# Kernel tuning notes

Hardware: AMD Instinct MI355X
Metric: run time of the kernel (lower is better)

Reference implementation:

```python
import jax, jax.numpy as jnp
import numpy as np
import math

B_, V_, D_, N_, H_, W_ = 4, 8, 64, 16, 32, 32
V_LIST = [0.0, 45.0, 90.0, 135.0, 180.0, 225.0, 270.0, 315.0]
GROUPS = 4
EPS = 1e-5


def _make_sample_coords():
    # Replicates F.affine_grid(align_corners=False) for fixed rotation matrices,
    # then maps normalized grid coords to input pixel coords as grid_sample does.
    xs = (np.arange(W_) + 0.5) * 2.0 / W_ - 1.0
    ys = (np.arange(H_) + 0.5) * 2.0 / H_ - 1.0
    X, Y = np.meshgrid(xs, ys)  # (H, W)
    ix_list, iy_list = [], []
    for w in V_LIST:
        a = math.radians(-w)
        c, s = math.cos(a), math.sin(a)
        gx = c * X - s * Y  # theta = [[c,-s,0],[s,c,0]]
        gy = s * X + c * Y
        ix_list.append((gx + 1.0) * W_ / 2.0 - 0.5)
        iy_list.append((gy + 1.0) * H_ / 2.0 - 0.5)
    return (jnp.asarray(np.stack(ix_list), jnp.float32),
            jnp.asarray(np.stack(iy_list), jnp.float32))

IX, IY = _make_sample_coords()  # each (V, H, W)


def _bilinear(sv, iy, ix):
    # sv: (B, D, N, H, W); iy, ix: (H, W) float sampling coords (pixel space)
    x0 = jnp.floor(ix)
    y0 = jnp.floor(iy)
    wx1 = ix - x0
    wy1 = iy - y0

    def corner(yc, xc, wgt):
        m = (yc >= 0) & (yc < H_) & (xc >= 0) & (xc < W_)  # zeros padding
        yi = jnp.clip(yc, 0, H_ - 1).astype(jnp.int32)
        xi = jnp.clip(xc, 0, W_ - 1).astype(jnp.int32)
        return sv[..., yi, xi] * jnp.where(m, wgt, 0.0)

    return (corner(y0, x0, (1.0 - wy1) * (1.0 - wx1))
            + corner(y0, x0 + 1.0, (1.0 - wy1) * wx1)
            + corner(y0 + 1.0, x0, wy1 * (1.0 - wx1))
            + corner(y0 + 1.0, x0 + 1.0, wy1 * wx1))

# vmap over the velocity axis V of s_prev and the per-velocity grids
_transport = jax.vmap(_bilinear, in_axes=(1, 0, 0), out_axes=1)


def _conv(x, w, b=None):
    y = jax.lax.conv_general_dilated(x, w, (1, 1), 'SAME',
                                     dimension_numbers=('NCHW', 'OIHW', 'NCHW'))
    if b is not None:
        y = y + b[None, :, None, None]
    return y


def _group_norm(x, w, b):
    Bn, D, H, W = x.shape
    xg = x.reshape(Bn, GROUPS, D // GROUPS, H, W)
    mu = xg.mean(axis=(2, 3, 4), keepdims=True)
    var = xg.var(axis=(2, 3, 4), keepdims=True)
    xn = ((xg - mu) * jax.lax.rsqrt(var + EPS)).reshape(Bn, D, H, W)
    return xn * w[None, :, None, None] + b[None, :, None, None]


def setup_inputs() -> dict:
    key = jax.random.key(0)
    ks = jax.random.split(key, 5)
    return {
        "u_t": jax.random.normal(ks[0], (B_, D_, H_, W_), jnp.float32),
        "s_prev": jax.random.normal(ks[1], (B_, V_, D_, N_, H_, W_), jnp.float32) * 0.1,
        "gn_w": jnp.ones((D_,), jnp.float32),
        "gn_b": jnp.zeros((D_,), jnp.float32),
        "conv_delta_w": jax.random.normal(ks[2], (D_, D_, 3, 3), jnp.float32) * 0.02,
        "conv_delta_b": jnp.zeros((D_,), jnp.float32),
        "conv_B_w": jax.random.normal(ks[3], (N_, D_, 3, 3), jnp.float32) * 0.02,
        "conv_C_w": jax.random.normal(ks[4], (N_, D_, 3, 3), jnp.float32) * 0.02,
        "log_A_real": jnp.full((D_, N_), math.log(0.5), jnp.float32),
        "D_param": jnp.ones((D_,), jnp.float32),
        "dt_bias": jnp.float32(math.log(math.e - 1.0)),
    }


def reference(u_t, s_prev, gn_w, gn_b, conv_delta_w, conv_delta_b,
              conv_B_w, conv_C_w, log_A_real, D_param, dt_bias):
    u_norm = _group_norm(u_t, gn_w, gn_b)
    delta = jax.nn.softplus(_conv(u_norm, conv_delta_w, conv_delta_b) + dt_bias)
    delta = jnp.clip(delta, 1e-4, 5.0)                               # (B,D,H,W)
    B_val = _conv(u_norm, conv_B_w)                                  # (B,N,H,W)
    C_val = _conv(u_norm, conv_C_w)                                  # (B,N,H,W)
    A = -jnp.exp(log_A_real)                                         # (D,N)
    A_bar = jnp.exp(delta[:, :, None] * A[None, :, :, None, None])   # (B,D,N,H,W)
    B_bar = delta[:, :, None] * B_val[:, None]                       # (B,D,N,H,W)
    s_trans = _transport(s_prev, IY, IX)                             # (B,V,D,N,H,W)
    s_new = A_bar[:, None] * s_trans + B_bar[:, None] * u_t[:, None, :, None]
    y_state = jnp.einsum('bvdnhw,bnhw->bvdhw', s_new, C_val)
    y_new = y_state + u_t[:, None] * D_param[None, None, :, None, None]
    return (y_new, s_new)
```

## Files before the change

kernel.cpp:

```cpp
#include <hip/hip_runtime.h>
#include <cmath>

#define FSQ 0.70710678118654752440f
__constant__ float CTAB[8] = {1.f,  FSQ, 0.f, -FSQ, -1.f, -FSQ, 0.f, FSQ};
__constant__ float STAB[8] = {0.f, -FSQ, -1.f, -FSQ,  0.f,  FSQ, 1.f, FSQ};

__global__ __launch_bounds__(256) void gn_kernel(const float* __restrict__ u,
                                                 const float* __restrict__ gw,
                                                 const float* __restrict__ gb,
                                                 float* __restrict__ up)
{
    int blk = blockIdx.x;
    int b = blk >> 2, g = blk & 3;
    int t = threadIdx.x;
    const float* src = u + ((size_t)(b * 64 + g * 16) << 10);
    float sum = 0.f, sq = 0.f;
    #pragma unroll
    for (int r = 0; r < 64; ++r) {
        float v = src[t + (r << 8)];
        sum += v; sq += v * v;
    }
    __shared__ float red[256], red2[256];
    red[t] = sum; red2[t] = sq;
    __syncthreads();
    for (int ofs = 128; ofs > 0; ofs >>= 1) {
        if (t < ofs) { red[t] += red[t + ofs]; red2[t] += red2[t + ofs]; }
        __syncthreads();
    }
    float mu  = red[0] * (1.f / 16384.f);
    float var = red2[0] * (1.f / 16384.f) - mu * mu;
    float rs  = rsqrtf(var + 1e-5f);

    float* pb = up + (size_t)(b * 64 + g * 16) * 1156;
    for (int k = t; k < 16 * 132; k += 256) {
        int pl = k / 132, c = k % 132;
        int idx;
        if (c < 34)       idx = c;
        else if (c < 68)  idx = 33 * 34 + (c - 34);
        else if (c < 100) idx = (c - 68 + 1) * 34;
        else              idx = (c - 100 + 1) * 34 + 33;
        pb[pl * 1156 + idx] = 0.f;
    }
    for (int r = 0; r < 64; ++r) {
        int idx = t + (r << 8);
        int ch = idx >> 10, rem = idx & 1023;
        int y = rem >> 5, x = rem & 31;
        float val = (src[idx] - mu) * rs * gw[g * 16 + ch] + gb[g * 16 + ch];
        pb[ch * 1156 + (y + 1) * 34 + (x + 1)] = val;
    }
}

__global__ __launch_bounds__(256) void conv_kernel(const float* __restrict__ up,
                                                   const float* __restrict__ wd,
                                                   const float* __restrict__ bd,
                                                   const float* __restrict__ wB,
                                                   const float* __restrict__ wC,
                                                   const float* __restrict__ dtb,
                                                   float* __restrict__ delta,
                                                   float* __restrict__ Bv,
                                                   float* __restrict__ Cv)
{
    int blk = blockIdx.x;
    int o = blk % 96, b = blk / 96;
    int t = threadIdx.x;
    int w = t & 31, h0 = (t >> 5) << 2;
    const float* wsel;
    if (o < 64)      wsel = wd + (size_t)o * 576;
    else if (o < 80) wsel = wB + (size_t)(o - 64) * 576;
    else             wsel = wC + (size_t)(o - 80) * 576;
    const float* plane = up + (size_t)b * 64 * 1156;

    float acc[4] = {0.f, 0.f, 0.f, 0.f};
    for (int ci = 0; ci < 64; ++ci) {
        const float* pl = plane + ci * 1156 + h0 * 34 + w;
        const float* wp = wsel + ci * 9;
        float v[6][3];
        #pragma unroll
        for (int ry = 0; ry < 6; ++ry)
            #pragma unroll
            for (int dx = 0; dx < 3; ++dx)
                v[ry][dx] = pl[ry * 34 + dx];
        float w9[9];
        #pragma unroll
        for (int k = 0; k < 9; ++k) w9[k] = wp[k];
        #pragma unroll
        for (int r = 0; r < 4; ++r)
            #pragma unroll
            for (int dy = 0; dy < 3; ++dy)
                #pragma unroll
                for (int dx = 0; dx < 3; ++dx)
                    acc[r] += v[r + dy][dx] * w9[dy * 3 + dx];
    }

    int pbase = (h0 << 5) + w;
    if (o < 64) {
        float bias = bd[o] + dtb[0];
        float* dst = delta + ((size_t)(b * 64 + o) << 10) + pbase;
        #pragma unroll
        for (int r = 0; r < 4; ++r) {
            float x = acc[r] + bias;
            float sp = (x > 20.f) ? x : log1pf(expf(x));
            sp = fminf(fmaxf(sp, 1e-4f), 5.f);
            dst[r << 5] = sp;
        }
    } else {
        float* dst = (o < 80) ? (Bv + ((size_t)(b * 16 + o - 64) << 10) + pbase)
                              : (Cv + ((size_t)(b * 16 + o - 80) << 10) + pbase);
        #pragma unroll
        for (int r = 0; r < 4; ++r) dst[r << 5] = acc[r];
    }
}

__global__ __launch_bounds__(256) void fused_state_kernel(
    const float* __restrict__ s_prev, const float* __restrict__ u_t,
    const float* __restrict__ delta, const float* __restrict__ Bv,
    const float* __restrict__ Cv, const float* __restrict__ logA,
    const float* __restrict__ Dp, float* __restrict__ y_out,
    float* __restrict__ s_out)
{
    __shared__ float lds[8516];
    __shared__ float Ash[16];
    int blk = blockIdx.x;
    int d = blk & 63, v = (blk >> 6) & 7, b = blk >> 9;
    int t = threadIdx.x;

    if (t < 16) Ash[t] = -expf(logA[d * 16 + t]);
    for (int k = t; k < 324; k += 256) {
        int idx;
        if (k < 34)       idx = k;
        else if (k < 290) { int q = k - 34; idx = 34 + (q >> 5) * 1056 + (q & 31) * 33 + 32; }
        else              idx = 8482 + (k - 290);
        lds[idx] = 0.f;
    }

    const float cc = CTAB[v], ss = STAB[v];
    const float* dpl = delta + ((size_t)(b * 64 + d) << 10);
    const float* upl = u_t   + ((size_t)(b * 64 + d) << 10);

    float w00[4], w01[4], w10[4], w11[4], du[4], dl[4], uu[4], yacc[4];
    int base[4];
    #pragma unroll
    for (int i = 0; i < 4; ++i) {
        int p = t + (i << 8);
        int h = p >> 5, wpx = p & 31;
        float X = (wpx + 0.5f) * 0.0625f - 1.f;
        float Y = (h + 0.5f) * 0.0625f - 1.f;
        float gx = cc * X - ss * Y;
        float gy = ss * X + cc * Y;
        float ix = (gx + 1.f) * 16.f - 0.5f;
        float iy = (gy + 1.f) * 16.f - 0.5f;
        float fx0 = floorf(ix), fy0 = floorf(iy);
        float wx = ix - fx0, wy = iy - fy0;
        int x0 = (int)fx0, y0 = (int)fy0;
        bool vx0 = (x0 >= 0) && (x0 < 32);
        bool vx1 = (x0 >= -1) && (x0 < 31);
        bool vy0 = (y0 >= 0) && (y0 < 32);
        bool vy1 = (y0 >= -1) && (y0 < 31);
        float mx0 = vx0 ? (1.f - wx) : 0.f;
        float mx1 = vx1 ? wx : 0.f;
        float my0 = vy0 ? (1.f - wy) : 0.f;
        float my1 = vy1 ? wy : 0.f;
        w00[i] = my0 * mx0; w01[i] = my0 * mx1;
        w10[i] = my1 * mx0; w11[i] = my1 * mx1;
        int bx = min(max(x0, -1), 31), by = min(max(y0, -1), 31);
        base[i] = 34 + by * 33 + bx;
        float dd = dpl[p], uv = upl[p];
        dl[i] = dd; uu[i] = uv; du[i] = dd * uv; yacc[i] = 0.f;
    }

    size_t so = ((size_t)((b * 8 + v) * 64 + d)) << 14;
    const float* sb  = s_prev + so;
    float* sob = s_out + so;
    const float* BvB = Bv + ((size_t)b << 14);
    const float* CvB = Cv + ((size_t)b << 14);

    for (int ch = 0; ch < 2; ++ch) {
        const float4* src = (const float4*)(sb + (ch << 13));
        #pragma unroll
        for (int q0 = 0; q0 < 8; ++q0) {
            int q = t + (q0 << 8);
            float4 val = src[q];
            int lin = q << 2;
            int n = lin >> 10, rem = lin & 1023;
            int di = 34 + n * 1056 + (rem >> 5) * 33 + (rem & 31);
            lds[di] = val.x; lds[di + 1] = val.y; lds[di + 2] = val.z; lds[di + 3] = val.w;
        }
        __syncthreads();

        const float* bvc = BvB + (ch << 13);
        const float* cvc = CvB + (ch << 13);
        float* soc = sob + (ch << 13);
        #pragma unroll
        for (int i = 0; i < 4; ++i) {
            int p = t + (i << 8);
            #pragma unroll
            for (int n = 0; n < 8; ++n) {
                int si = base[i] + n * 1056;
                float s00 = lds[si], s01 = lds[si + 1];
                float s10 = lds[si + 33], s11 = lds[si + 34];
                float bil = s00 * w00[i] + s01 * w01[i] + s10 * w10[i] + s11 * w11[i];
                float abar = __expf(dl[i] * Ash[(ch << 3) + n]);
                float sn = abar * bil + du[i] * bvc[(n << 10) + p];
                soc[(n << 10) + p] = sn;
                yacc[i] += sn * cvc[(n << 10) + p];
            }
        }
        __syncthreads();
    }

    float Dd = Dp[d];
    float* yo = y_out + (((size_t)((b * 8 + v) * 64 + d)) << 10);
    #pragma unroll
    for (int i = 0; i < 4; ++i) {
        int p = t + (i << 8);
        yo[p] = yacc[i] + uu[i] * Dd;
    }
}

extern "C" void kernel_launch(void* const* d_in, const int* in_sizes, int n_in,
                              void* d_out, int out_size, void* d_ws, size_t ws_size,
                              hipStream_t stream)
{
    const float* u_t    = (const float*)d_in[0];
    const float* s_prev = (const float*)d_in[1];
    const float* gn_w   = (const float*)d_in[2];
    const float* gn_b   = (const float*)d_in[3];
    const float* wd     = (const float*)d_in[4];
    const float* bd     = (const float*)d_in[5];
    const float* wB     = (const float*)d_in[6];
    const float* wC     = (const float*)d_in[7];
    const float* logA   = (const float*)d_in[8];
    const float* Dp     = (const float*)d_in[9];
    const float* dtb    = (const float*)d_in[10];

    float* y_out = (float*)d_out;
    float* s_out = y_out + 2097152;

    float* up    = (float*)d_ws;
    float* delta = up + 295936;
    float* Bv    = delta + 262144;
    float* Cv    = Bv + 65536;

    hipLaunchKernelGGL(gn_kernel, dim3(16), dim3(256), 0, stream, u_t, gn_w, gn_b, up);
    hipLaunchKernelGGL(conv_kernel, dim3(384), dim3(256), 0, stream,
                       up, wd, bd, wB, wC, dtb, delta, Bv, Cv);
    hipLaunchKernelGGL(fused_state_kernel, dim3(2048), dim3(256), 0, stream,
                       s_prev, u_t, delta, Bv, Cv, logA, Dp, y_out, s_out);
}
```

Measured before the change: 346.5 us.

## Split conv into row strips with LDS staging and split state kernel over N

The conv kernel now launches one block per (batch, output channel, 4-row strip), stages the 6-row halo of all 64 input channels in shared memory, and splits the input-channel sum across two thread halves that are reduced through LDS. The fused state kernel is split into two blocks per (b,v,d), each handling 8 of the 16 state channels with a 34-wide padded LDS tile. The partial y sums are combined with atomicAdd into an output that is first zeroed by a memset. The aim is more parallelism and occupancy in both kernels, at the cost of an extra memset pass, atomic traffic on y, and repeated loading of the conv input per output channel.

```diff
diff --git a/kernel.cpp b/kernel.cpp
--- a/kernel.cpp
+++ b/kernel.cpp
@@ -60,54 +60,60 @@
                                                    float* __restrict__ Bv,
                                                    float* __restrict__ Cv)
 {
+    __shared__ float sin_[64 * 204];
+    __shared__ float red[256];
     int blk = blockIdx.x;
-    int o = blk % 96, b = blk / 96;
+    int strip = blk & 7;
+    int o = (blk >> 3) & 127; o = o % 96;
+    o = ((blk >> 3) - (blk / 768) * 96);
+    int b = blk / 768;
+    int h0 = strip * 4;
     int t = threadIdx.x;
-    int w = t & 31, h0 = (t >> 5) << 2;
+
+    const float* plane = up + (size_t)b * 73984;
+    for (int idx = t; idx < 13056; idx += 256) {
+        int ci = idx / 204;
+        int rem = idx - ci * 204;
+        sin_[idx] = plane[ci * 1156 + h0 * 34 + rem];
+    }
+    __syncthreads();
+
     const float* wsel;
     if (o < 64)      wsel = wd + (size_t)o * 576;
     else if (o < 80) wsel = wB + (size_t)(o - 64) * 576;
     else             wsel = wC + (size_t)(o - 80) * 576;
-    const float* plane = up + (size_t)b * 64 * 1156;
-
-    float acc[4] = {0.f, 0.f, 0.f, 0.f};
-    for (int ci = 0; ci < 64; ++ci) {
-        const float* pl = plane + ci * 1156 + h0 * 34 + w;
+
+    int half = t >> 7;
+    int px = t & 127;
+    int r = px >> 5, c = px & 31;
+    const float* base = sin_ + r * 34 + c;
+
+    float acc = 0.f;
+    int ci0 = half * 32;
+    for (int ci = ci0; ci < ci0 + 32; ++ci) {
+        const float* pp = base + ci * 204;
         const float* wp = wsel + ci * 9;
-        float v[6][3];
         #pragma unroll
-        for (int ry = 0; ry < 6; ++ry)
+        for (int dy = 0; dy < 3; ++dy)
             #pragma unroll
             for (int dx = 0; dx < 3; ++dx)
-                v[ry][dx] = pl[ry * 34 + dx];
-        float w9[9];
-        #pragma unroll
-        for (int k = 0; k < 9; ++k) w9[k] = wp[k];
-        #pragma unroll
-        for (int r = 0; r < 4; ++r)
-            #pragma unroll
-            for (int dy = 0; dy < 3; ++dy)
-                #pragma unroll
-                for (int dx = 0; dx < 3; ++dx)
-                    acc[r] += v[r + dy][dx] * w9[dy * 3 + dx];
-    }
-
-    int pbase = (h0 << 5) + w;
-    if (o < 64) {
-        float bias = bd[o] + dtb[0];
-        float* dst = delta + ((size_t)(b * 64 + o) << 10) + pbase;
-        #pragma unroll
-        for (int r = 0; r < 4; ++r) {
-            float x = acc[r] + bias;
+                acc += pp[dy * 34 + dx] * wp[dy * 3 + dx];
+    }
+    red[t] = acc;
+    __syncthreads();
+    if (t < 128) {
+        float a = red[t] + red[t + 128];
+        int pidx = (h0 + r) * 32 + c;
+        if (o < 64) {
+            float x = a + bd[o] + dtb[0];
             float sp = (x > 20.f) ? x : log1pf(expf(x));
             sp = fminf(fmaxf(sp, 1e-4f), 5.f);
-            dst[r << 5] = sp;
+            delta[((size_t)(b * 64 + o) << 10) + pidx] = sp;
+        } else if (o < 80) {
+            Bv[((size_t)(b * 16 + o - 64) << 10) + pidx] = a;
+        } else {
+            Cv[((size_t)(b * 16 + o - 80) << 10) + pidx] = a;
         }
-    } else {
-        float* dst = (o < 80) ? (Bv + ((size_t)(b * 16 + o - 64) << 10) + pbase)
-                              : (Cv + ((size_t)(b * 16 + o - 80) << 10) + pbase);
-        #pragma unroll
-        for (int r = 0; r < 4; ++r) dst[r << 5] = acc[r];
     }
 }
 
@@ -118,28 +124,47 @@
     const float* __restrict__ Dp, float* __restrict__ y_out,
     float* __restrict__ s_out)
 {
-    __shared__ float lds[8516];
-    __shared__ float Ash[16];
+    __shared__ float lds[8 * 1156];
+    __shared__ float Ash[8];
     int blk = blockIdx.x;
-    int d = blk & 63, v = (blk >> 6) & 7, b = blk >> 9;
+    int cchunk = blk & 1;
+    int d = (blk >> 1) & 63, v = (blk >> 7) & 7, b = blk >> 10;
     int t = threadIdx.x;
 
-    if (t < 16) Ash[t] = -expf(logA[d * 16 + t]);
-    for (int k = t; k < 324; k += 256) {
+    if (t < 8) Ash[t] = -__expf(logA[d * 16 + cchunk * 8 + t]);
+    for (int k = t; k < 1056; k += 256) {
+        int pl = k >> 7; int g = k & 127;
+        pl = k / 132; g = k - pl * 132;
         int idx;
-        if (k < 34)       idx = k;
-        else if (k < 290) { int q = k - 34; idx = 34 + (q >> 5) * 1056 + (q & 31) * 33 + 32; }
-        else              idx = 8482 + (k - 290);
-        lds[idx] = 0.f;
-    }
+        if (g < 34)       idx = g;
+        else if (g < 68)  idx = 1122 + (g - 34);
+        else if (g < 100) idx = (g - 67) * 34;
+        else              idx = (g - 99) * 34 + 33;
+        lds[pl * 1156 + idx] = 0.f;
+    }
+
+    size_t so = (((size_t)((b * 8 + v) * 64 + d)) << 14) + (cchunk << 13);
+    const float4* src = (const float4*)(s_prev + so);
+    #pragma unroll
+    for (int k = 0; k < 8; ++k) {
+        int q = t + (k << 8);
+        float4 val = src[q];
+        int lin = q << 2;
+        int nn = lin >> 10, rem = lin & 1023;
+        int di = nn * 1156 + ((rem >> 5) + 1) * 34 + (rem & 31) + 1;
+        lds[di] = val.x; lds[di + 1] = val.y; lds[di + 2] = val.z; lds[di + 3] = val.w;
+    }
+    __syncthreads();
 
     const float cc = CTAB[v], ss = STAB[v];
     const float* dpl = delta + ((size_t)(b * 64 + d) << 10);
     const float* upl = u_t   + ((size_t)(b * 64 + d) << 10);
-
-    float w00[4], w01[4], w10[4], w11[4], du[4], dl[4], uu[4], yacc[4];
-    int base[4];
-    #pragma unroll
+    const float* bvc = Bv + ((size_t)b << 14) + (cchunk << 13);
+    const float* cvc = Cv + ((size_t)b << 14) + (cchunk << 13);
+    float* soc = s_out + so;
+    float* yo  = y_out + (((size_t)((b * 8 + v) * 64 + d)) << 10);
+    float Dd = Dp[d];
+
     for (int i = 0; i < 4; ++i) {
         int p = t + (i << 8);
         int h = p >> 5, wpx = p & 31;
@@ -152,68 +177,32 @@
         float fx0 = floorf(ix), fy0 = floorf(iy);
         float wx = ix - fx0, wy = iy - fy0;
         int x0 = (int)fx0, y0 = (int)fy0;
-        bool vx0 = (x0 >= 0) && (x0 < 32);
-        bool vx1 = (x0 >= -1) && (x0 < 31);
-        bool vy0 = (y0 >= 0) && (y0 < 32);
-        bool vy1 = (y0 >= -1) && (y0 < 31);
-        float mx0 = vx0 ? (1.f - wx) : 0.f;
-        float mx1 = vx1 ? wx : 0.f;
-        float my0 = vy0 ? (1.f - wy) : 0.f;
-        float my1 = vy1 ? wy : 0.f;
-        w00[i] = my0 * mx0; w01[i] = my0 * mx1;
-        w10[i] = my1 * mx0; w11[i] = my1 * mx1;
+        float mx0 = (x0 >= 0 && x0 < 32) ? (1.f - wx) : 0.f;
+        float mx1 = (x0 >= -1 && x0 < 31) ? wx : 0.f;
+        float my0 = (y0 >= 0 && y0 < 32) ? (1.f - wy) : 0.f;
+        float my1 = (y0 >= -1 && y0 < 31) ? wy : 0.f;
+        float w00 = my0 * mx0, w01 = my0 * mx1;
+        float w10 = my1 * mx0, w11 = my1 * mx1;
         int bx = min(max(x0, -1), 31), by = min(max(y0, -1), 31);
-        base[i] = 34 + by * 33 + bx;
+        int base = (by + 1) * 34 + (bx + 1);
+
         float dd = dpl[p], uv = upl[p];
-        dl[i] = dd; uu[i] = uv; du[i] = dd * uv; yacc[i] = 0.f;
-    }
-
-    size_t so = ((size_t)((b * 8 + v) * 64 + d)) << 14;
-    const float* sb  = s_prev + so;
-    float* sob = s_out + so;
-    const float* BvB = Bv + ((size_t)b << 14);
-    const float* CvB = Cv + ((size_t)b << 14);
-
-    for (int ch = 0; ch < 2; ++ch) {
-        const float4* src = (const float4*)(sb + (ch << 13));
+        float du = dd * uv;
+        float yacc = 0.f;
         #pragma unroll
-        for (int q0 = 0; q0 < 8; ++q0) {
-            int q = t + (q0 << 8);
-            float4 val = src[q];
-            int lin = q << 2;
-            int n = lin >> 10, rem = lin & 1023;
-            int di = 34 + n * 1056 + (rem >> 5) * 33 + (rem & 31);
-            lds[di] = val.x; lds[di + 1] = val.y; lds[di + 2] = val.z; lds[di + 3] = val.w;
+        for (int nn = 0; nn < 8; ++nn) {
+            int si = base + nn * 1156;
+            float s00 = lds[si], s01 = lds[si + 1];
+            float s10 = lds[si + 34], s11 = lds[si + 35];
+            float bil = s00 * w00 + s01 * w01 + s10 * w10 + s11 * w11;
+            float abar = __expf(dd * Ash[nn]);
+            float bvv = bvc[(nn << 10) + p];
+            float sn = abar * bil + du * bvv;
+            soc[(nn << 10) + p] = sn;
+            yacc += sn * cvc[(nn << 10) + p];
         }
-        __syncthreads();
-
-        const float* bvc = BvB + (ch << 13);
-        const float* cvc = CvB + (ch << 13);
-        float* soc = sob + (ch << 13);
-        #pragma unroll
-        for (int i = 0; i < 4; ++i) {
-            int p = t + (i << 8);
-            #pragma unroll
-            for (int n = 0; n < 8; ++n) {
-                int si = base[i] + n * 1056;
-                float s00 = lds[si], s01 = lds[si + 1];
-                float s10 = lds[si + 33], s11 = lds[si + 34];
-                float bil = s00 * w00[i] + s01 * w01[i] + s10 * w10[i] + s11 * w11[i];
-                float abar = __expf(dl[i] * Ash[(ch << 3) + n]);
-                float sn = abar * bil + du[i] * bvc[(n << 10) + p];
-                soc[(n << 10) + p] = sn;
-                yacc[i] += sn * cvc[(n << 10) + p];
-            }
-        }
-        __syncthreads();
-    }
-
-    float Dd = Dp[d];
-    float* yo = y_out + (((size_t)((b * 8 + v) * 64 + d)) << 10);
-    #pragma unroll
-    for (int i = 0; i < 4; ++i) {
-        int p = t + (i << 8);
-        yo[p] = yacc[i] + uu[i] * Dd;
+        float val = yacc + (cchunk == 0 ? uv * Dd : 0.f);
+        atomicAdd(yo + p, val);
     }
 }
 
@@ -241,9 +230,11 @@
     float* Bv    = delta + 262144;
     float* Cv    = Bv + 65536;
 
+    hipMemsetAsync(y_out, 0, (size_t)2097152 * sizeof(float), stream);
+
     hipLaunchKernelGGL(gn_kernel, dim3(16), dim3(256), 0, stream, u_t, gn_w, gn_b, up);
-    hipLaunchKernelGGL(conv_kernel, dim3(384), dim3(256), 0, stream,
+    hipLaunchKernelGGL(conv_kernel, dim3(3072), dim3(256), 0, stream,
                        up, wd, bd, wB, wC, dtb, delta, Bv, Cv);
-    hipLaunchKernelGGL(fused_state_kernel, dim3(2048), dim3(256), 0, stream,
+    hipLaunchKernelGGL(fused_state_kernel, dim3(4096), dim3(256), 0, stream,
                        s_prev, u_t, delta, Bv, Cv, logA, Dp, y_out, s_out);
 }
```

Result: faster. 319.3 us (-7.8%).
